# Performance work log

Measured on AMD Instinct MI355X. Metric: run time of the kernel, lower is better.

## Reference

```python
import jax, jax.numpy as jnp
import numpy as np

B, C, N = 2, 128, 4096
BN_EPS = 1e-5


def setup_inputs() -> dict:
    key = jax.random.key(0)
    ks = jax.random.split(key, 16)
    Ch, Cd = C // 2, C // 8

    def bn_params(k1, c):
        k1, k2 = jax.random.split(k1)
        return (1.0 + 0.1 * jax.random.normal(k1, (c,), jnp.float32),  # gamma
                0.1 * jax.random.normal(k2, (c,), jnp.float32),        # beta
                jnp.zeros((c,), jnp.float32),                          # running mean
                jnp.ones((c,), jnp.float32))                           # running var

    g1, be1, m1, v1 = bn_params(ks[4], Ch)
    g2, be2, m2, v2 = bn_params(ks[5], Ch)
    gu, beu, mu, vu = bn_params(ks[6], C)
    return {
        "xyz": jax.random.normal(ks[0], (B, 3, N), jnp.float32),
        "features": jax.random.normal(ks[1], (B, C, N), jnp.float32),
        "w_mlp1": 0.1 * jax.random.normal(ks[2], (Ch, 6), jnp.float32),
        "b_mlp1": jnp.zeros((Ch,), jnp.float32),
        "g_mlp1": g1, "be_mlp1": be1, "m_mlp1": m1, "v_mlp1": v1,
        "w_mlp2": 0.05 * jax.random.normal(ks[3], (Ch, 2 * C), jnp.float32),
        "b_mlp2": jnp.zeros((Ch,), jnp.float32),
        "g_mlp2": g2, "be_mlp2": be2, "m_mlp2": m2, "v_mlp2": v2,
        "w_down1": 0.1 * jax.random.normal(ks[7], (Cd, C), jnp.float32),
        "w_down2": 0.1 * jax.random.normal(ks[8], (Cd, C), jnp.float32),
        "w_up": 0.1 * jax.random.normal(ks[9], (C, Cd), jnp.float32),
        "b_up": jnp.zeros((C,), jnp.float32),
        "g_up": gu, "be_up": beu, "m_up": mu, "v_up": vu,
        "k": 20,
    }


def _knn_idx(x, k):
    # x: [B,3,N]; pairwise_distance = -||xi-xj||^2, topk -> nearest
    xx = jnp.sum(x * x, axis=1)                       # [B,N]
    inner = jnp.einsum('bcn,bcm->bnm', x, x)          # [B,N,N]
    pd = 2.0 * inner - xx[:, :, None] - xx[:, None, :]
    return jax.lax.top_k(pd, k)[1]                    # [B,N,k]


def _gather_edge(feat_t, idx):
    # feat_t: [B,N,C], idx: [B,N,k] -> concat(nbr - center, center): [B,N,k,2C]
    nbr = jax.vmap(lambda a, i: a[i])(feat_t, idx)    # [B,N,k,C]
    center = feat_t[:, :, None, :]
    center_b = jnp.broadcast_to(center, nbr.shape)
    return jnp.concatenate((nbr - center, center_b), axis=-1)


def _bn(x, g, b, m, v, ch_axis=1):
    shape = [1] * x.ndim
    shape[ch_axis] = -1
    r = lambda p: p.reshape(shape)
    return (x - r(m)) * (r(g) / jnp.sqrt(r(v) + BN_EPS)) + r(b)


def reference(xyz, features, w_mlp1, b_mlp1, g_mlp1, be_mlp1, m_mlp1, v_mlp1,
              w_mlp2, b_mlp2, g_mlp2, be_mlp2, m_mlp2, v_mlp2,
              w_down1, w_down2, w_up, b_up, g_up, be_up, m_up, v_up, k):
    idx = _knn_idx(xyz, k)
    edge_x = _gather_edge(jnp.swapaxes(xyz, 1, 2), idx)        # [B,N,k,6]
    edge_f = _gather_edge(jnp.swapaxes(features, 1, 2), idx)   # [B,N,k,2C]

    # 1x1 conv2d + BN + ReLU on both branches (channels last via einsum)
    h1 = jnp.einsum('bnkc,oc->bonk', edge_x, w_mlp1) + b_mlp1[None, :, None, None]
    h1 = jax.nn.relu(_bn(h1, g_mlp1, be_mlp1, m_mlp1, v_mlp1))
    h2 = jnp.einsum('bnkc,oc->bonk', edge_f, w_mlp2) + b_mlp2[None, :, None, None]
    h2 = jax.nn.relu(_bn(h2, g_mlp2, be_mlp2, m_mlp2, v_mlp2))

    f_enc = jnp.max(jnp.concatenate((h1, h2), axis=1), axis=-1)  # [B,C,N]

    f1 = jax.nn.relu(jnp.einsum('bcn,oc->bon', f_enc, w_down1))  # [B,C/8,N]
    f2 = jax.nn.relu(jnp.einsum('bcn,oc->bon', f_enc, w_down2))

    # NOTE: original code indexes [0] after mean -> uses batch element 0 only
    f_channel = jnp.mean(f1, axis=-1, keepdims=True)[0]          # [C/8,1]
    f_space = jnp.mean(f2, axis=1, keepdims=True)[0]             # [1,N]
    final = jnp.sqrt(f_channel @ f_space + 1e-12)                # [C/8,N]
    final = final[None] + f1 + f2                                # [B,C/8,N]

    up = jnp.einsum('bcn,oc->bon', final, w_up) + b_up[None, :, None]
    final = jax.nn.relu(_bn(up, g_up, be_up, m_up, v_up))        # [B,C,N]

    f_local = f_enc - final
    return f_local * jnp.tanh(jax.nn.softplus(f_local))          # Mish
```

## Files before the change

### kernel.cpp

```cpp
#include <hip/hip_runtime.h>
#include <hip/hip_bf16.h>

#define BB 2
#define CC 128
#define NN 4096
#define KK 20

#define WS_FLAG   0
#define WS_FCACC  16
#define WS_S1     32
#define WS_C1     96
#define WS_S2     160
#define WS_C2     224
#define WS_SUP    288
#define WS_CUP    416
#define WS_FS     1024
#define WS_X      8192
#define WS_XX     32768
#define WS_W1     40960
#define WS_W2T    41344
#define WS_WD1    57728
#define WS_WD2    59776
#define WS_WUP    61824
#define WS_P      65536
#define WS_Q      1114112
#define WS_FE     2326528
#define WS_F12    3375104

struct InPtrs { const void* p[22]; };

__device__ __forceinline__ int detect_bf16(const void* xyz) {
  const unsigned* u = (const unsigned*)xyz;
  int cnt = 0;
  for (int i = 0; i < 64; ++i) {
    unsigned lo = u[i] & 0x7FFFu;
    cnt += (lo >= 0x3C00u && lo <= 0x4100u) ? 1 : 0;
  }
  return cnt >= 32;
}

__device__ __forceinline__ float ldin(const void* p, long long i, int flag) {
  if (flag) {
    unsigned short b = ((const unsigned short*)p)[i];
    return __uint_as_float(((unsigned)b) << 16);
  }
  return ((const float*)p)[i];
}

__device__ __forceinline__ unsigned sortable(float v) {
  unsigned u = __float_as_uint(v);
  return (u & 0x80000000u) ? ~u : (u | 0x80000000u);
}

__device__ __forceinline__ unsigned wave_max_u32(unsigned x) {
  unsigned t;
  t = (unsigned)__builtin_amdgcn_update_dpp(0, (int)x, 0x111, 0xF, 0xF, true); x = x > t ? x : t;
  t = (unsigned)__builtin_amdgcn_update_dpp(0, (int)x, 0x112, 0xF, 0xF, true); x = x > t ? x : t;
  t = (unsigned)__builtin_amdgcn_update_dpp(0, (int)x, 0x114, 0xF, 0xF, true); x = x > t ? x : t;
  t = (unsigned)__builtin_amdgcn_update_dpp(0, (int)x, 0x118, 0xF, 0xF, true); x = x > t ? x : t;
  t = (unsigned)__builtin_amdgcn_update_dpp(0, (int)x, 0x142, 0xF, 0xF, true); x = x > t ? x : t;
  t = (unsigned)__builtin_amdgcn_update_dpp(0, (int)x, 0x143, 0xF, 0xF, true); x = x > t ? x : t;
  return (unsigned)__builtin_amdgcn_readlane((int)x, 63);
}

__device__ __forceinline__ void insert4p(unsigned pd, int idx,
    unsigned& p0, int& i0, unsigned& p1, int& i1,
    unsigned& p2, int& i2, unsigned& p3, int& i3) {
  bool b0 = pd > p0, b1 = pd > p1, b2 = pd > p2, b3 = pd > p3;
  p3 = b3 ? (b2 ? p2 : pd) : p3;  i3 = b3 ? (b2 ? i2 : idx) : i3;
  p2 = b2 ? (b1 ? p1 : pd) : p2;  i2 = b2 ? (b1 ? i1 : idx) : i2;
  p1 = b1 ? (b0 ? p0 : pd) : p1;  i1 = b1 ? (b0 ? i0 : idx) : i1;
  p0 = b0 ? pd : p0;              i0 = b0 ? idx : i0;
}

__global__ __launch_bounds__(256) void k0_convert(InPtrs in, float* ws) {
  int flag = detect_bf16(in.p[0]);
  int gid = blockIdx.x * 256 + threadIdx.x;
  int stride = gridDim.x * 256;
  for (int i = gid; i < 16384; i += stride) {
    int c = i >> 6, o = i & 63;
    ws[WS_W2T + i] = ldin(in.p[8], o * 256 + c, flag);
  }
  const int T0 = 24576;
  const int T1 = T0 + 384;
  const int T2 = T1 + 2048;
  const int T3 = T2 + 2048;
  const int T4 = T3 + 2048;
  for (int i = gid; i < T4; i += stride) {
    const void* src; int off, dst;
    if      (i < T0) { src = in.p[0];  off = i;      dst = WS_X   + off; }
    else if (i < T1) { src = in.p[2];  off = i - T0; dst = WS_W1  + off; }
    else if (i < T2) { src = in.p[14]; off = i - T1; dst = WS_WD1 + off; }
    else if (i < T3) { src = in.p[15]; off = i - T2; dst = WS_WD2 + off; }
    else             { src = in.p[16]; off = i - T3; dst = WS_WUP + off; }
    ws[dst] = ldin(src, off, flag);
  }
  if (blockIdx.x == 0) {
    int t = threadIdx.x;
    if (t < 64) {
      float b1 = ldin(in.p[3], t, flag), g1 = ldin(in.p[4], t, flag);
      float be1 = ldin(in.p[5], t, flag), m1 = ldin(in.p[6], t, flag), v1 = ldin(in.p[7], t, flag);
      float s1 = g1 / sqrtf(v1 + 1e-5f);
      ws[WS_S1 + t] = s1;
      ws[WS_C1 + t] = s1 * (b1 - m1) + be1;
      float b2 = ldin(in.p[9], t, flag), g2 = ldin(in.p[10], t, flag);
      float be2 = ldin(in.p[11], t, flag), m2 = ldin(in.p[12], t, flag), v2 = ldin(in.p[13], t, flag);
      float s2 = g2 / sqrtf(v2 + 1e-5f);
      ws[WS_S2 + t] = s2;
      ws[WS_C2 + t] = s2 * (b2 - m2) + be2;
    }
    if (t < 128) {
      float bu = ldin(in.p[17], t, flag), gu = ldin(in.p[18], t, flag);
      float beu = ldin(in.p[19], t, flag), mu = ldin(in.p[20], t, flag), vu = ldin(in.p[21], t, flag);
      float su = gu / sqrtf(vu + 1e-5f);
      ws[WS_SUP + t] = su;
      ws[WS_CUP + t] = su * (bu - mu) + beu;
    }
    if (t < 16) ws[WS_FCACC + t] = 0.f;
    if (t == 0) ((int*)ws)[WS_FLAG] = flag;
  }
}

__global__ __launch_bounds__(256) void k1_pq(InPtrs in, float* ws) {
  int t = threadIdx.x;
  int bid = blockIdx.x;
  int b = bid >> 9;
  int mt = (bid >> 3) & 63;
  int ot = bid & 7;
  int w = __builtin_amdgcn_readfirstlane(t >> 6);
  int lane = t & 63;
  int o0 = ot * 8 + w * 2;
  int m = (mt << 6) + lane;
  int flag = ((const int*)ws)[WS_FLAG];
  const float* W2T = ws + WS_W2T;
  float accP[2] = {0.f, 0.f}, accQ[2] = {0.f, 0.f};
  long long fb = (long long)b * CC * NN + m;
#define K1_BODY(FVAL)                                            \
    {                                                            \
      float f = (FVAL);                                          \
      accP[0] = fmaf(W2T[c * 64 + o0 + 0], f, accP[0]);          \
      accP[1] = fmaf(W2T[c * 64 + o0 + 1], f, accP[1]);          \
      accQ[0] = fmaf(W2T[(128 + c) * 64 + o0 + 0], f, accQ[0]);  \
      accQ[1] = fmaf(W2T[(128 + c) * 64 + o0 + 1], f, accQ[1]);  \
    }
  if (flag) {
    const unsigned short* F = (const unsigned short*)in.p[1] + fb;
#pragma unroll 8
    for (int c = 0; c < 128; ++c)
      K1_BODY(__uint_as_float(((unsigned)F[(long long)c * NN]) << 16))
  } else {
    const float* F = (const float*)in.p[1] + fb;
#pragma unroll 8
    for (int c = 0; c < 128; ++c)
      K1_BODY(F[(long long)c * NN])
  }
#undef K1_BODY
  const float* X = ws + WS_X + (long long)b * 3 * NN;
  float x0 = X[m], x1 = X[NN + m], x2 = X[2 * NN + m];
  const float* W1 = ws + WS_W1;
  float* P = ws + WS_P + ((long long)(b * NN + m)) * 128;
  float* Q = ws + WS_Q + ((long long)(b * NN + m)) * 128;
  float2 p1v, q1v, p2v, q2v;
#pragma unroll
  for (int j = 0; j < 2; ++j) {
    int o = o0 + j;
    float s1 = ws[WS_S1 + o], c1 = ws[WS_C1 + o];
    float px = fmaf(W1[o * 6 + 2], x2, fmaf(W1[o * 6 + 1], x1, W1[o * 6 + 0] * x0));
    float qx = fmaf(W1[o * 6 + 5], x2, fmaf(W1[o * 6 + 4], x1, W1[o * 6 + 3] * x0));
    (&p1v.x)[j] = s1 * px;
    (&q1v.x)[j] = fmaf(s1, qx - px, c1);
    float s2 = ws[WS_S2 + o], c2 = ws[WS_C2 + o];
    (&p2v.x)[j] = s2 * accP[j];
    (&q2v.x)[j] = fmaf(s2, accQ[j] - accP[j], c2);
  }
  *(float2*)(P + o0)      = p1v;
  *(float2*)(P + 64 + o0) = p2v;
  *(float2*)(Q + o0)      = q1v;
  *(float2*)(Q + 64 + o0) = q2v;
  if (ot == 0 && w == 0) {
    float xx = __fadd_rn(__fadd_rn(__fmul_rn(x0, x0), __fmul_rn(x1, x1)), __fmul_rn(x2, x2));
    ws[WS_XX + b * NN + m] = xx;
  }
}

__global__ __launch_bounds__(256) void k23_knn_fenc(float* ws) {
  int t = threadIdx.x;
  int w = t >> 6, lane = t & 63;
  int pt = blockIdx.x * 4 + w;
  int b = pt >> 12;
  int n = pt & (NN - 1);
  const float* X = ws + WS_X + (long long)b * 3 * NN;
  const float* XX = ws + WS_XX + (long long)b * NN;
  float xc0 = X[n], xc1 = X[NN + n], xc2 = X[2 * NN + n], xxn = XX[n];
  unsigned p0 = 0, p1 = 0, p2 = 0, p3 = 0;
  int i0 = 0, i1 = 0, i2 = 0, i3 = 0;
#pragma unroll 8
  for (int s = 0; s < 64; ++s) {
    int m = s * 64 + lane;
    float c0 = X[m], c1 = X[NN + m], c2 = X[2 * NN + m], xxm = XX[m];
    float inner = __fadd_rn(__fadd_rn(__fmul_rn(c0, xc0), __fmul_rn(c1, xc1)), __fmul_rn(c2, xc2));
    float pd = __fsub_rn(__fsub_rn(__fmul_rn(2.0f, inner), xxn), xxm);
    insert4p(sortable(pd), m, p0, i0, p1, i1, p2, i2, p3, i3);
  }
  unsigned long long used = 0;
  int nv = 4;
  int winner = 0;
  for (int r = 0; r < KK; ++r) {
    unsigned spd = wave_max_u32(p0);
    unsigned long long msk = __ballot(p0 == spd);
    int sidx;
    if (__popcll(msk) == 1) {
      sidx = __builtin_amdgcn_readlane(i0, (int)(__ffsll((long long)msk) - 1));
    } else {
      unsigned cand = (p0 == spd) ? (unsigned)(4095 - i0) : 0u;
      sidx = (int)(4095u - wave_max_u32(cand));
    }
    if (lane == r) winner = sidx;
    if (p0 == spd && i0 == sidx) {
      used |= 1ull << (i0 >> 6);
      p0 = p1; i0 = i1; p1 = p2; i1 = i2; p2 = p3; i2 = i3; p3 = 0; i3 = 0;
      if (--nv == 0) {
        p0 = p1 = p2 = p3 = 0; i0 = i1 = i2 = i3 = 0;
#pragma unroll 1
        for (int s = 0; s < 64; ++s) {
          if (!((used >> s) & 1ull)) {
            int m = s * 64 + lane;
            float c0 = X[m], c1 = X[NN + m], c2 = X[2 * NN + m], xxm = XX[m];
            float inner = __fadd_rn(__fadd_rn(__fmul_rn(c0, xc0), __fmul_rn(c1, xc1)), __fmul_rn(c2, xc2));
            float pd = __fsub_rn(__fsub_rn(__fmul_rn(2.0f, inner), xxn), xxm);
            insert4p(sortable(pd), m, p0, i0, p1, i1, p2, i2, p3, i3);
          }
        }
        nv = 4;
      }
    }
  }
  const float* Q = ws + WS_Q + (long long)pt * 128;
  const float* Pb = ws + WS_P + (long long)b * NN * 128;
  float2 q = ((const float2*)Q)[lane];
  int ids[KK];
#pragma unroll
  for (int j = 0; j < KK; ++j) ids[j] = __shfl(winner, j);
  float mx0 = -3.4e38f, mx1 = -3.4e38f;
#pragma unroll
  for (int j = 0; j < KK; ++j) {
    float2 p = ((const float2*)(Pb + (long long)ids[j] * 128))[lane];
    mx0 = fmaxf(mx0, p.x + q.x);
    mx1 = fmaxf(mx1, p.y + q.y);
  }
  float2 fe = make_float2(fmaxf(mx0, 0.f), fmaxf(mx1, 0.f));
  ((float2*)(ws + WS_FE + (long long)pt * 128))[lane] = fe;
}

__global__ __launch_bounds__(256) void k4_down(float* ws) {
  __shared__ float ldsFE[8 * 128];
  __shared__ float ldsW[32 * 129];
  __shared__ float ldsFC[16];
  int t = threadIdx.x;
  int b = blockIdx.x >> 9;
  int n0 = (blockIdx.x & 511) << 3;
  for (int i = t; i < 8 * 128; i += 256) {
    int p = i >> 7, c = i & 127;
    ldsFE[i] = ws[WS_FE + (long long)(b * NN + n0 + p) * 128 + c];
  }
  for (int i = t; i < 32 * 128; i += 256) {
    int o = i >> 7, c = i & 127;
    ldsW[o * 129 + c] = (o < 16) ? ws[WS_WD1 + o * 128 + c] : ws[WS_WD2 + (o - 16) * 128 + c];
  }
  if (t < 16) ldsFC[t] = 0.f;
  __syncthreads();
  int p = t >> 5, oid = t & 31;
  float acc = 0.f;
#pragma unroll 8
  for (int c = 0; c < 128; ++c)
    acc = fmaf(ldsW[oid * 129 + c], ldsFE[p * 128 + c], acc);
  float v = fmaxf(acc, 0.f);
  ws[WS_F12 + (long long)(b * NN + n0 + p) * 32 + oid] = v;
  if (b == 0) {
    if (oid >= 16) {
      float s = v;
#pragma unroll
      for (int d = 1; d < 16; d <<= 1) s += __shfl_xor(s, d);
      if (oid == 16) ws[WS_FS + n0 + p] = s * 0.0625f;
    } else {
      atomicAdd(&ldsFC[oid], v);
    }
  }
  __syncthreads();
  if (b == 0 && t < 16) atomicAdd(ws + WS_FCACC + t, ldsFC[t]);
}

__global__ __launch_bounds__(256) void k5_final(float* ws, float* outf, __hip_bfloat16* outb) {
  __shared__ float fin[16 * 16];
  int t = threadIdx.x;
  int g = t >> 4;
  int p = t & 15;
  int b = blockIdx.x >> 8;
  int n0 = (blockIdx.x & 255) << 4;
  int n = n0 + p;
  int flag = ((const int*)ws)[WS_FLAG];
  {
    float fs = ws[WS_FS + n];
    float fc = ws[WS_FCACC + g] * (1.0f / NN);
    float f1v = ws[WS_F12 + (long long)(b * NN + n) * 32 + g];
    float f2v = ws[WS_F12 + (long long)(b * NN + n) * 32 + 16 + g];
    fin[p * 16 + g] = sqrtf(fc * fs + 1e-12f) + f1v + f2v;
  }
  __syncthreads();
  const float4* FE4 = (const float4*)(ws + WS_FE + (long long)(b * NN + n) * 128 + g * 8);
  float fev[8];
  {
    float4 a = FE4[0], c = FE4[1];
    fev[0] = a.x; fev[1] = a.y; fev[2] = a.z; fev[3] = a.w;
    fev[4] = c.x; fev[5] = c.y; fev[6] = c.z; fev[7] = c.w;
  }
#pragma unroll
  for (int j = 0; j < 8; ++j) {
    int o = g * 8 + j;
    float acc = 0.f;
#pragma unroll
    for (int c = 0; c < 16; ++c)
      acc = fmaf(ws[WS_WUP + o * 16 + c], fin[p * 16 + c], acc);
    float fo = fmaf(ws[WS_SUP + o], acc, ws[WS_CUP + o]);
    fo = fmaxf(fo, 0.f);
    float fl = fev[j] - fo;
    float u = __expf(fl);
    float nmr = u * (u + 2.f);
    float y = fl * __fdividef(nmr, nmr + 2.f);
    if (fl > 15.f) y = fl;
    long long oi = ((long long)b * CC + o) * NN + n;
    if (flag) outb[oi] = __float2bfloat16(y);
    else      outf[oi] = y;
  }
}

extern "C" void kernel_launch(void* const* d_in, const int* in_sizes, int n_in,
                              void* d_out, int out_size, void* d_ws, size_t ws_size,
                              hipStream_t stream) {
  (void)in_sizes; (void)out_size; (void)ws_size;
  float* ws = (float*)d_ws;
  InPtrs ip;
  for (int i = 0; i < 22; ++i) ip.p[i] = (i < n_in) ? d_in[i] : nullptr;
  hipLaunchKernelGGL(k0_convert,   dim3(128),          dim3(256), 0, stream, ip, ws);
  hipLaunchKernelGGL(k1_pq,        dim3(1024),         dim3(256), 0, stream, ip, ws);
  hipLaunchKernelGGL(k23_knn_fenc, dim3(BB * NN / 4),  dim3(256), 0, stream, ws);
  hipLaunchKernelGGL(k4_down,      dim3(BB * NN / 8),  dim3(256), 0, stream, ws);
  hipLaunchKernelGGL(k5_final,     dim3(BB * NN / 16), dim3(256), 0, stream, ws,
                     (float*)d_out, (__hip_bfloat16*)d_out);
}
```

Measured before the change: 195.6 us.

## Fold input conversion kernel into k1_pq and stage W2 rows in LDS

Removes the separate k0_convert launch. Its work moves into k1_pq: the first 128 blocks copy xyz and the down/up weights into the workspace, and block 0 computes the up-BN constants. Each block detects bf16 with a wave ballot, loads its 8 rows of w_mlp2 into shared memory in interleaved P/Q order, and reads mlp1 weights, BN params and xyz straight from the inputs. This saves a launch and a dependent pass, at the cost of a redundant W2 load and BN-constant recomputation in every block.

```diff
diff --git a/kernel.cpp b/kernel.cpp
--- a/kernel.cpp
+++ b/kernel.cpp
@@ -8,17 +8,11 @@
 
 #define WS_FLAG   0
 #define WS_FCACC  16
-#define WS_S1     32
-#define WS_C1     96
-#define WS_S2     160
-#define WS_C2     224
 #define WS_SUP    288
 #define WS_CUP    416
 #define WS_FS     1024
 #define WS_X      8192
 #define WS_XX     32768
-#define WS_W1     40960
-#define WS_W2T    41344
 #define WS_WD1    57728
 #define WS_WD2    59776
 #define WS_WUP    61824
@@ -28,16 +22,6 @@
 #define WS_F12    3375104
 
 struct InPtrs { const void* p[22]; };
-
-__device__ __forceinline__ int detect_bf16(const void* xyz) {
-  const unsigned* u = (const unsigned*)xyz;
-  int cnt = 0;
-  for (int i = 0; i < 64; ++i) {
-    unsigned lo = u[i] & 0x7FFFu;
-    cnt += (lo >= 0x3C00u && lo <= 0x4100u) ? 1 : 0;
-  }
-  return cnt >= 32;
-}
 
 __device__ __forceinline__ float ldin(const void* p, long long i, int flag) {
   if (flag) {
@@ -73,75 +57,57 @@
   p0 = b0 ? pd : p0;              i0 = b0 ? idx : i0;
 }
 
-__global__ __launch_bounds__(256) void k0_convert(InPtrs in, float* ws) {
-  int flag = detect_bf16(in.p[0]);
-  int gid = blockIdx.x * 256 + threadIdx.x;
-  int stride = gridDim.x * 256;
-  for (int i = gid; i < 16384; i += stride) {
-    int c = i >> 6, o = i & 63;
-    ws[WS_W2T + i] = ldin(in.p[8], o * 256 + c, flag);
-  }
-  const int T0 = 24576;
-  const int T1 = T0 + 384;
-  const int T2 = T1 + 2048;
-  const int T3 = T2 + 2048;
-  const int T4 = T3 + 2048;
-  for (int i = gid; i < T4; i += stride) {
-    const void* src; int off, dst;
-    if      (i < T0) { src = in.p[0];  off = i;      dst = WS_X   + off; }
-    else if (i < T1) { src = in.p[2];  off = i - T0; dst = WS_W1  + off; }
-    else if (i < T2) { src = in.p[14]; off = i - T1; dst = WS_WD1 + off; }
-    else if (i < T3) { src = in.p[15]; off = i - T2; dst = WS_WD2 + off; }
-    else             { src = in.p[16]; off = i - T3; dst = WS_WUP + off; }
-    ws[dst] = ldin(src, off, flag);
-  }
-  if (blockIdx.x == 0) {
-    int t = threadIdx.x;
-    if (t < 64) {
-      float b1 = ldin(in.p[3], t, flag), g1 = ldin(in.p[4], t, flag);
-      float be1 = ldin(in.p[5], t, flag), m1 = ldin(in.p[6], t, flag), v1 = ldin(in.p[7], t, flag);
-      float s1 = g1 / sqrtf(v1 + 1e-5f);
-      ws[WS_S1 + t] = s1;
-      ws[WS_C1 + t] = s1 * (b1 - m1) + be1;
-      float b2 = ldin(in.p[9], t, flag), g2 = ldin(in.p[10], t, flag);
-      float be2 = ldin(in.p[11], t, flag), m2 = ldin(in.p[12], t, flag), v2 = ldin(in.p[13], t, flag);
-      float s2 = g2 / sqrtf(v2 + 1e-5f);
-      ws[WS_S2 + t] = s2;
-      ws[WS_C2 + t] = s2 * (b2 - m2) + be2;
-    }
-    if (t < 128) {
-      float bu = ldin(in.p[17], t, flag), gu = ldin(in.p[18], t, flag);
-      float beu = ldin(in.p[19], t, flag), mu = ldin(in.p[20], t, flag), vu = ldin(in.p[21], t, flag);
-      float su = gu / sqrtf(vu + 1e-5f);
-      ws[WS_SUP + t] = su;
-      ws[WS_CUP + t] = su * (bu - mu) + beu;
-    }
-    if (t < 16) ws[WS_FCACC + t] = 0.f;
-    if (t == 0) ((int*)ws)[WS_FLAG] = flag;
-  }
-}
-
 __global__ __launch_bounds__(256) void k1_pq(InPtrs in, float* ws) {
+  __shared__ float ldsW2[8 * 128 * 2];
   int t = threadIdx.x;
   int bid = blockIdx.x;
   int b = bid >> 9;
   int mt = (bid >> 3) & 63;
   int ot = bid & 7;
+  int lane = t & 63;
+  unsigned xw = ((const unsigned*)in.p[0])[lane];
+  unsigned lo = xw & 0x7FFFu;
+  unsigned long long bm = __ballot(lo >= 0x3C00u && lo <= 0x4100u);
+  int flag = (__popcll(bm) >= 32) ? 1 : 0;
+  for (int i = t; i < 2048; i += 256) {
+    int r = i >> 8, cc = i & 255;
+    ldsW2[((r * 128 + (cc & 127)) << 1) + (cc >> 7)] =
+        ldin(in.p[8], (ot * 8 + r) * 256 + cc, flag);
+  }
+  if (bid < 128) {
+    int gid = bid * 256 + t;
+    if      (gid < 24576) ws[WS_X   + gid]         = ldin(in.p[0],  gid,         flag);
+    else if (gid < 26624) ws[WS_WD1 + gid - 24576] = ldin(in.p[14], gid - 24576, flag);
+    else if (gid < 28672) ws[WS_WD2 + gid - 26624] = ldin(in.p[15], gid - 26624, flag);
+    else if (gid < 30720) ws[WS_WUP + gid - 28672] = ldin(in.p[16], gid - 28672, flag);
+    if (bid == 0) {
+      if (t < 128) {
+        float bu = ldin(in.p[17], t, flag), gu = ldin(in.p[18], t, flag);
+        float beu = ldin(in.p[19], t, flag), mu = ldin(in.p[20], t, flag), vu = ldin(in.p[21], t, flag);
+        float su = gu / sqrtf(vu + 1e-5f);
+        ws[WS_SUP + t] = su;
+        ws[WS_CUP + t] = su * (bu - mu) + beu;
+      }
+      if (t < 16) ws[WS_FCACC + t] = 0.f;
+      if (t == 0) ((int*)ws)[WS_FLAG] = flag;
+    }
+  }
+  __syncthreads();
   int w = __builtin_amdgcn_readfirstlane(t >> 6);
-  int lane = t & 63;
   int o0 = ot * 8 + w * 2;
   int m = (mt << 6) + lane;
-  int flag = ((const int*)ws)[WS_FLAG];
-  const float* W2T = ws + WS_W2T;
+  const float2* w2r0 = (const float2*)ldsW2 + (w * 2) * 128;
+  const float2* w2r1 = (const float2*)ldsW2 + (w * 2 + 1) * 128;
   float accP[2] = {0.f, 0.f}, accQ[2] = {0.f, 0.f};
   long long fb = (long long)b * CC * NN + m;
-#define K1_BODY(FVAL)                                            \
-    {                                                            \
-      float f = (FVAL);                                          \
-      accP[0] = fmaf(W2T[c * 64 + o0 + 0], f, accP[0]);          \
-      accP[1] = fmaf(W2T[c * 64 + o0 + 1], f, accP[1]);          \
-      accQ[0] = fmaf(W2T[(128 + c) * 64 + o0 + 0], f, accQ[0]);  \
-      accQ[1] = fmaf(W2T[(128 + c) * 64 + o0 + 1], f, accQ[1]);  \
+#define K1_BODY(FVAL)                                  \
+    {                                                  \
+      float f = (FVAL);                                \
+      float2 v0 = w2r0[c], v1 = w2r1[c];               \
+      accP[0] = fmaf(v0.x, f, accP[0]);                \
+      accQ[0] = fmaf(v0.y, f, accQ[0]);                \
+      accP[1] = fmaf(v1.x, f, accP[1]);                \
+      accQ[1] = fmaf(v1.y, f, accQ[1]);                \
     }
   if (flag) {
     const unsigned short* F = (const unsigned short*)in.p[1] + fb;
@@ -155,21 +121,31 @@
       K1_BODY(F[(long long)c * NN])
   }
 #undef K1_BODY
-  const float* X = ws + WS_X + (long long)b * 3 * NN;
-  float x0 = X[m], x1 = X[NN + m], x2 = X[2 * NN + m];
-  const float* W1 = ws + WS_W1;
+  long long xb = (long long)b * 3 * NN;
+  float x0 = ldin(in.p[0], xb + m, flag);
+  float x1 = ldin(in.p[0], xb + NN + m, flag);
+  float x2 = ldin(in.p[0], xb + 2 * NN + m, flag);
   float* P = ws + WS_P + ((long long)(b * NN + m)) * 128;
   float* Q = ws + WS_Q + ((long long)(b * NN + m)) * 128;
   float2 p1v, q1v, p2v, q2v;
 #pragma unroll
   for (int j = 0; j < 2; ++j) {
     int o = o0 + j;
-    float s1 = ws[WS_S1 + o], c1 = ws[WS_C1 + o];
-    float px = fmaf(W1[o * 6 + 2], x2, fmaf(W1[o * 6 + 1], x1, W1[o * 6 + 0] * x0));
-    float qx = fmaf(W1[o * 6 + 5], x2, fmaf(W1[o * 6 + 4], x1, W1[o * 6 + 3] * x0));
+    float b1 = ldin(in.p[3], o, flag), g1 = ldin(in.p[4], o, flag);
+    float be1 = ldin(in.p[5], o, flag), m1 = ldin(in.p[6], o, flag), v1 = ldin(in.p[7], o, flag);
+    float s1 = g1 / sqrtf(v1 + 1e-5f);
+    float c1 = s1 * (b1 - m1) + be1;
+    float b2 = ldin(in.p[9], o, flag), g2 = ldin(in.p[10], o, flag);
+    float be2 = ldin(in.p[11], o, flag), m2 = ldin(in.p[12], o, flag), v2 = ldin(in.p[13], o, flag);
+    float s2 = g2 / sqrtf(v2 + 1e-5f);
+    float c2 = s2 * (b2 - m2) + be2;
+    float w10 = ldin(in.p[2], o * 6 + 0, flag), w11 = ldin(in.p[2], o * 6 + 1, flag);
+    float w12 = ldin(in.p[2], o * 6 + 2, flag), w13 = ldin(in.p[2], o * 6 + 3, flag);
+    float w14 = ldin(in.p[2], o * 6 + 4, flag), w15 = ldin(in.p[2], o * 6 + 5, flag);
+    float px = fmaf(w12, x2, fmaf(w11, x1, w10 * x0));
+    float qx = fmaf(w15, x2, fmaf(w14, x1, w13 * x0));
     (&p1v.x)[j] = s1 * px;
     (&q1v.x)[j] = fmaf(s1, qx - px, c1);
-    float s2 = ws[WS_S2 + o], c2 = ws[WS_C2 + o];
     (&p2v.x)[j] = s2 * accP[j];
     (&q2v.x)[j] = fmaf(s2, accQ[j] - accP[j], c2);
   }
@@ -341,7 +317,6 @@
   float* ws = (float*)d_ws;
   InPtrs ip;
   for (int i = 0; i < 22; ++i) ip.p[i] = (i < n_in) ? d_in[i] : nullptr;
-  hipLaunchKernelGGL(k0_convert,   dim3(128),          dim3(256), 0, stream, ip, ws);
   hipLaunchKernelGGL(k1_pq,        dim3(1024),         dim3(256), 0, stream, ip, ws);
   hipLaunchKernelGGL(k23_knn_fenc, dim3(BB * NN / 4),  dim3(256), 0, stream, ws);
   hipLaunchKernelGGL(k4_down,      dim3(BB * NN / 8),  dim3(256), 0, stream, ws);
```

Measured after the change: 190.9 us. 1.02x faster.
